# Kernel tuning notes

Measured on AMD Instinct MI355X. Metric: run time of the kernel, lower is better.

The kernel has to match this reference:

```python
import jax, jax.numpy as jnp
import numpy as np

WS = 4          # window size per axis
HEADS = 3
HEAD_DIM = 32
DIM = 96
DISP = WS // 2  # displacement for shifted windows


def _make_mask(axis):
    # (w^3, w^3) additive mask, -inf across the wrap-around boundary on `axis`
    m = np.zeros((WS, WS, WS, WS, WS, WS), dtype=np.float32)
    d = DISP
    if axis == 0:
        m[-d:, :, :, :-d, :, :] = -np.inf
        m[:-d, :, :, -d:, :, :] = -np.inf
    elif axis == 1:
        m[:, -d:, :, :, :-d, :] = -np.inf
        m[:, :-d, :, :, -d:, :] = -np.inf
    else:
        m[:, :, -d:, :, :, :-d] = -np.inf
        m[:, :, :-d, :, :, -d:] = -np.inf
    return jnp.asarray(m.reshape(WS**3, WS**3))


def setup_inputs() -> dict:
    key = jax.random.key(0)
    k1, k2, k3, k4 = jax.random.split(key, 4)
    inner = HEADS * HEAD_DIM
    x = jax.random.normal(k1, (1, 64, 64, 64, DIM), dtype=jnp.float32)
    w_qkv = jax.random.normal(k2, (3 * inner, DIM), dtype=jnp.float32) * 0.02
    w_out = jax.random.normal(k3, (DIM, inner), dtype=jnp.float32) * 0.02
    b_out = jax.random.normal(k4, (DIM,), dtype=jnp.float32) * 0.02
    return {
        'x': x, 'w_qkv': w_qkv, 'w_out': w_out, 'b_out': b_out,
        'x_mask': _make_mask(0), 'y_mask': _make_mask(1), 'z_mask': _make_mask(2),
    }


def _forward(x, w_qkv, w_out, b_out, x_mask, y_mask, z_mask):
    scale = HEAD_DIM ** -0.5
    b, nx, ny, nz, _ = x.shape
    nwx, nwy, nwz = nx // WS, ny // WS, nz // WS
    seq = WS ** 3
    # cyclic shift by -displacement
    x = jnp.roll(x, shift=(-DISP, -DISP, -DISP), axis=(1, 2, 3))
    qkv = jnp.einsum('bxyzc,oc->bxyzo', x, w_qkv)
    q, k, v = jnp.split(qkv, 3, axis=-1)

    def win(t):  # -> (b, h, n_windows, seq, d)
        t = t.reshape(b, nwx, WS, nwy, WS, nwz, WS, HEADS, HEAD_DIM)
        t = t.transpose(0, 7, 1, 3, 5, 2, 4, 6, 8)
        return t.reshape(b, HEADS, nwx * nwy * nwz, seq, HEAD_DIM)

    q, k, v = win(q), win(k), win(v)
    dots = jnp.einsum('bhwid,bhwjd->bhwij', q, k) * scale

    # shifted-window masking (faithful to original einops relabeling, incl.
    # the final mislabeled rearrange which permutes the window grid)
    d = dots.reshape(b, HEADS, nwx, nwy, nwz, seq, seq)
    d = d.transpose(0, 1, 3, 4, 2, 5, 6)          # (b,h,ny,nz,nx,i,j)
    d = d.at[:, :, :, :, -1].add(x_mask)
    d = d.transpose(0, 1, 4, 3, 2, 5, 6)          # (b,h,nx,nz,ny,i,j)
    d = d.at[:, :, :, :, -1].add(y_mask)
    d = d.transpose(0, 1, 2, 4, 3, 5, 6)          # (b,h,nx,ny,nz,i,j)
    d = d.transpose(0, 1, 4, 2, 3, 5, 6)          # original's final rearrange bug
    dots = d.reshape(b, HEADS, nwx * nwy * nwz, seq, seq)

    attn = jax.nn.softmax(dots, axis=-1)
    out = jnp.einsum('bhwij,bhwjd->bhwid', attn, v)
    # un-window
    out = out.reshape(b, HEADS, nwx, nwy, nwz, WS, WS, WS, HEAD_DIM)
    out = out.transpose(0, 2, 5, 3, 6, 4, 7, 1, 8).reshape(b, nx, ny, nz, HEADS * HEAD_DIM)
    out = jnp.einsum('bxyzc,oc->bxyzo', out, w_out) + b_out
    # cyclic back shift
    return jnp.roll(out, shift=(DISP, DISP, DISP), axis=(1, 2, 3))


def reference(x, w_qkv, w_out, b_out, x_mask, y_mask, z_mask):
    return _forward(x, w_qkv, w_out, b_out, x_mask, y_mask, z_mask)
```

## Files before the change

kernel.cpp:

```cpp
#include <hip/hip_runtime.h>
#include <hip/hip_bf16.h>


using bf4   = __attribute__((ext_vector_type(4))) short;
using bf8   = __attribute__((ext_vector_type(8))) short;
using f32x4 = __attribute__((ext_vector_type(4))) float;

#define SW      104
#define WQ_ROWS 288
#define W_ROWS  384
#define W_SHORTS (W_ROWS * SW)

__device__ __forceinline__ short f2b(float f) {
  __hip_bfloat16 h = __float2bfloat16(f);
  return *reinterpret_cast<short*>(&h);
}
__device__ __forceinline__ bf4 pk4(const f32x4& a) {
  bf4 s; s[0] = f2b(a[0]); s[1] = f2b(a[1]); s[2] = f2b(a[2]); s[3] = f2b(a[3]);
  return s;
}
__device__ __forceinline__ bf4 pk4s(const f32x4& a, float sc) {
  bf4 s; s[0] = f2b(a[0] * sc); s[1] = f2b(a[1] * sc);
  s[2] = f2b(a[2] * sc); s[3] = f2b(a[3] * sc);
  return s;
}
__device__ __forceinline__ bf8 cvt8(const float4& a, const float4& b) {
  bf8 o;
  o[0] = f2b(a.x); o[1] = f2b(a.y); o[2] = f2b(a.z); o[3] = f2b(a.w);
  o[4] = f2b(b.x); o[5] = f2b(b.y); o[6] = f2b(b.z); o[7] = f2b(b.w);
  return o;
}

#if __has_builtin(__builtin_amdgcn_mfma_f32_16x16x16bf16_1k)
__device__ __forceinline__ f32x4 mfma16(bf4 a, bf4 b, f32x4 c) {
  return __builtin_amdgcn_mfma_f32_16x16x16bf16_1k(a, b, c, 0, 0, 0);
}
#elif __has_builtin(__builtin_amdgcn_mfma_f32_16x16x16_bf16)
__device__ __forceinline__ f32x4 mfma16(bf4 a, bf4 b, f32x4 c) {
  return __builtin_amdgcn_mfma_f32_16x16x16_bf16(a, b, c, 0, 0, 0);
}
#else
__device__ __forceinline__ f32x4 mfma16(bf4 a, bf4 b, f32x4 c) {
  asm("v_mfma_f32_16x16x16_bf16 %0, %1, %2, %0" : "+v"(c) : "v"(a), "v"(b));
  return c;
}
#endif

__global__ void prep_weights(const float* __restrict__ wq, const float* __restrict__ wo,
                             short* __restrict__ wpk) {
  int i = blockIdx.x * 256 + threadIdx.x;
  if (i >= W_SHORTS) return;
  int row = i / SW, c = i - row * SW;
  const float QS = 0.17677669529663687f;
  float v = 0.f;
  if (c < 96) {
    if (row < 96)           v = wq[row * 96 + c] * QS;
    else if (row < WQ_ROWS) v = wq[row * 96 + c];
    else                    v = wo[(row - WQ_ROWS) * 96 + c];
  }
  wpk[i] = f2b(v);
}

__global__ __launch_bounds__(512, 2)
void fused_swin3d(const float* __restrict__ x,
                  const short* __restrict__ wpk,
                  const float* __restrict__ bo,
                  float* __restrict__ out) {
  __shared__ __align__(16) short ls_w[W_SHORTS];

  const int tid = threadIdx.x;
  const float4* wsrc = reinterpret_cast<const float4*>(wpk);
  #pragma unroll
  for (int i = 0; i < 10; ++i) {
    int c = i * 512 + tid;
    if (c < W_SHORTS / 8)
      *reinterpret_cast<float4*>(&ls_w[c * 8]) = wsrc[c];
  }

  const int w = (int)blockIdx.x * 8 + (tid >> 6);
  const int p = w >> 8, q = (w >> 4) & 15, r = w & 15;
  const int lane = tid & 63;
  const int lr   = lane & 15;
  const int kg   = lane >> 4;
  const int sy = (lr >> 2) & 3, sz = lr & 3;
  const int ch0 = kg * 8;
  const short* ls_wo = ls_w + WQ_ROWS * SW;

  __syncthreads();

  bf4 qn[4][6], kn[4][6], vn[4][6];
  #pragma unroll
  for (int sc = 0; sc < 4; ++sc) {
    const int gx1 = (q * 4 + sc + 2) & 63, gy1 = (r * 4 + sy + 2) & 63, gz1 = (p * 4 + sz + 2) & 63;
    const int gx2 = (p * 4 + sc + 2) & 63, gy2 = (q * 4 + sy + 2) & 63, gz2 = (r * 4 + sz + 2) & 63;
    const size_t b1 = (size_t)((gx1 * 64 + gy1) * 64 + gz1) * 96;
    const size_t b2 = (size_t)((gx2 * 64 + gy2) * 64 + gz2) * 96;

    float4 xa0 = *reinterpret_cast<const float4*>(&x[b1 +  0 + ch0]);
    float4 xa1 = *reinterpret_cast<const float4*>(&x[b1 + 32 + ch0]);
    float4 xa2 = *reinterpret_cast<const float4*>(&x[b1 + 64 + ch0]);
    float4 xa3 = *reinterpret_cast<const float4*>(&x[b1 +  0 + ch0 + 4]);
    float4 xa4 = *reinterpret_cast<const float4*>(&x[b1 + 32 + ch0 + 4]);
    float4 xa5 = *reinterpret_cast<const float4*>(&x[b1 + 64 + ch0 + 4]);
    float4 xb0 = *reinterpret_cast<const float4*>(&x[b2 +  0 + ch0]);
    float4 xb1 = *reinterpret_cast<const float4*>(&x[b2 + 32 + ch0]);
    float4 xb2 = *reinterpret_cast<const float4*>(&x[b2 + 64 + ch0]);
    float4 xb3 = *reinterpret_cast<const float4*>(&x[b2 +  0 + ch0 + 4]);
    float4 xb4 = *reinterpret_cast<const float4*>(&x[b2 + 32 + ch0 + 4]);
    float4 xb5 = *reinterpret_cast<const float4*>(&x[b2 + 64 + ch0 + 4]);

    bf8 x1[3], x2[3];
    x1[0] = cvt8(xa0, xa3); x1[1] = cvt8(xa1, xa4); x1[2] = cvt8(xa2, xa5);
    x2[0] = cvt8(xb0, xb3); x2[1] = cvt8(xb1, xb4); x2[2] = cvt8(xb2, xb5);

    #pragma unroll
    for (int n = 0; n < 12; ++n) {
      f32x4 acc = {0.f, 0.f, 0.f, 0.f};
      const short* wrow = &ls_w[(n * 16 + lr) * SW + ch0];
      acc = __builtin_amdgcn_mfma_f32_16x16x32_bf16(*reinterpret_cast<const bf8*>(wrow +  0), x1[0], acc, 0, 0, 0);
      acc = __builtin_amdgcn_mfma_f32_16x16x32_bf16(*reinterpret_cast<const bf8*>(wrow + 32), x1[1], acc, 0, 0, 0);
      acc = __builtin_amdgcn_mfma_f32_16x16x32_bf16(*reinterpret_cast<const bf8*>(wrow + 64), x1[2], acc, 0, 0, 0);
      if (n < 6) qn[sc][n] = pk4(acc);
      else       kn[sc][n - 6] = pk4(acc);
    }
    #pragma unroll
    for (int n = 0; n < 6; ++n) {
      f32x4 acc = {0.f, 0.f, 0.f, 0.f};
      const short* wrow = &ls_w[(192 + n * 16 + lr) * SW + ch0];
      acc = __builtin_amdgcn_mfma_f32_16x16x32_bf16(x2[0], *reinterpret_cast<const bf8*>(wrow +  0), acc, 0, 0, 0);
      acc = __builtin_amdgcn_mfma_f32_16x16x32_bf16(x2[1], *reinterpret_cast<const bf8*>(wrow + 32), acc, 0, 0, 0);
      acc = __builtin_amdgcn_mfma_f32_16x16x32_bf16(x2[2], *reinterpret_cast<const bf8*>(wrow + 64), acc, 0, 0, 0);
      vn[sc][n] = pk4(acc);
    }
  }

  const bool mx = (q == 15), my = (r == 15);
  const bool killy = my && ((lr >= 8) != (kg >= 2));
  bf4 ob[4][6];

  #pragma unroll
  for (int qc = 0; qc < 4; ++qc) {
    f32x4 osw[6];
    #pragma unroll
    for (int c = 0; c < 6; ++c) osw[c] = (f32x4){0.f, 0.f, 0.f, 0.f};

    #pragma unroll
    for (int h = 0; h < 3; ++h) {
      f32x4 sv[4];
      #pragma unroll
      for (int nj = 0; nj < 4; ++nj) {
        f32x4 z = {0.f, 0.f, 0.f, 0.f};
        z = mfma16(kn[nj][2 * h + 0], qn[qc][2 * h + 0], z);
        sv[nj] = mfma16(kn[nj][2 * h + 1], qn[qc][2 * h + 1], z);
      }
      float sum = 0.f;
      #pragma unroll
      for (int nj = 0; nj < 4; ++nj) {
        const bool kill = killy || (mx && ((qc >= 2) != (nj >= 2)));
        #pragma unroll
        for (int t = 0; t < 4; ++t) {
          float ev = kill ? 0.f : __expf(sv[nj][t]);
          sv[nj][t] = ev;
          sum += ev;
        }
      }
      sum += __shfl_xor(sum, 16);
      sum += __shfl_xor(sum, 32);
      const float inv = 1.f / sum;
      bf4 pb[4];
      #pragma unroll
      for (int t = 0; t < 4; ++t) pb[t] = pk4s(sv[t], inv);
      #pragma unroll
      for (int nc = 0; nc < 2; ++nc)
        #pragma unroll
        for (int t = 0; t < 4; ++t)
          osw[2 * h + nc] = mfma16(vn[t][2 * h + nc], pb[t], osw[2 * h + nc]);
    }
    #pragma unroll
    for (int c = 0; c < 6; ++c) ob[qc][c] = pk4(osw[c]);
  }

  #pragma unroll
  for (int no = 0; no < 6; ++no) {
    bf4 wa[6];
    #pragma unroll
    for (int c = 0; c < 6; ++c)
      wa[c] = *reinterpret_cast<const bf4*>(&ls_wo[(no * 16 + lr) * SW + c * 16 + kg * 4]);
    const float4 bb = *reinterpret_cast<const float4*>(&bo[no * 16 + kg * 4]);
    #pragma unroll
    for (int qc = 0; qc < 4; ++qc) {
      f32x4 acc = {0.f, 0.f, 0.f, 0.f};
      #pragma unroll
      for (int c = 0; c < 6; ++c) acc = mfma16(wa[c], ob[qc][c], acc);
      const int gx2 = (p * 4 + qc + 2) & 63, gy2 = (q * 4 + sy + 2) & 63, gz2 = (r * 4 + sz + 2) & 63;
      const size_t b2 = (size_t)((gx2 * 64 + gy2) * 64 + gz2) * 96;
      float4 o4;
      o4.x = acc[0] + bb.x; o4.y = acc[1] + bb.y;
      o4.z = acc[2] + bb.z; o4.w = acc[3] + bb.w;
      *reinterpret_cast<float4*>(&out[b2 + no * 16 + kg * 4]) = o4;
    }
  }
}

extern "C" void kernel_launch(void* const* d_in, const int* in_sizes, int n_in,
                              void* d_out, int out_size, void* d_ws, size_t ws_size,
                              hipStream_t stream) {
  const float* x  = (const float*)d_in[0];
  const float* wq = (const float*)d_in[1];
  const float* wo = (const float*)d_in[2];
  const float* bo = (const float*)d_in[3];

  short* wpk = (short*)d_ws;

  prep_weights<<<(W_SHORTS + 255) / 256, 256, 0, stream>>>(wq, wo, wpk);
  fused_swin3d<<<512, 512, 0, stream>>>(x, wpk, bo, (float*)d_out);
}
```

Before: 109.2 us.

## Batch x loads per window and reuse weight fragments across spatial chunks

Each wave now issues all x loads for its four spatial chunks up front, then loops over output tiles and reuses each weight fragment read from LDS across the four chunks instead of rereading it per chunk. Blocks shrink from 512 to 256 threads with twice as many blocks, and the LDS row stride drops from 104 to 100 shorts. The intent is better memory-level parallelism and fewer LDS reads, and it also lowers LDS footprint per block so more blocks fit per CU. The cost is much higher register pressure from holding 24 float4 loads at once, which risks spills or lower occupancy.

```diff
diff --git a/kernel.cpp b/kernel.cpp
--- a/kernel.cpp
+++ b/kernel.cpp
@@ -6,7 +6,7 @@
 using bf8   = __attribute__((ext_vector_type(8))) short;
 using f32x4 = __attribute__((ext_vector_type(4))) float;
 
-#define SW      104
+#define SW      100
 #define WQ_ROWS 288
 #define W_ROWS  384
 #define W_SHORTS (W_ROWS * SW)
@@ -61,7 +61,8 @@
   wpk[i] = f2b(v);
 }
 
-__global__ __launch_bounds__(512, 2)
+__global__ __launch_bounds__(256)
+__attribute__((amdgpu_waves_per_eu(1, 2)))
 void fused_swin3d(const float* __restrict__ x,
                   const short* __restrict__ wpk,
                   const float* __restrict__ bo,
@@ -71,13 +72,13 @@
   const int tid = threadIdx.x;
   const float4* wsrc = reinterpret_cast<const float4*>(wpk);
   #pragma unroll
-  for (int i = 0; i < 10; ++i) {
-    int c = i * 512 + tid;
+  for (int i = 0; i < 19; ++i) {
+    int c = i * 256 + tid;
     if (c < W_SHORTS / 8)
       *reinterpret_cast<float4*>(&ls_w[c * 8]) = wsrc[c];
   }
 
-  const int w = (int)blockIdx.x * 8 + (tid >> 6);
+  const int w = (int)blockIdx.x * 4 + (tid >> 6);
   const int p = w >> 8, q = (w >> 4) & 15, r = w & 15;
   const int lane = tid & 63;
   const int lr   = lane & 15;
@@ -89,48 +90,76 @@
   __syncthreads();
 
   bf4 qn[4][6], kn[4][6], vn[4][6];
-  #pragma unroll
-  for (int sc = 0; sc < 4; ++sc) {
-    const int gx1 = (q * 4 + sc + 2) & 63, gy1 = (r * 4 + sy + 2) & 63, gz1 = (p * 4 + sz + 2) & 63;
-    const int gx2 = (p * 4 + sc + 2) & 63, gy2 = (q * 4 + sy + 2) & 63, gz2 = (r * 4 + sz + 2) & 63;
-    const size_t b1 = (size_t)((gx1 * 64 + gy1) * 64 + gz1) * 96;
-    const size_t b2 = (size_t)((gx2 * 64 + gy2) * 64 + gz2) * 96;
-
-    float4 xa0 = *reinterpret_cast<const float4*>(&x[b1 +  0 + ch0]);
-    float4 xa1 = *reinterpret_cast<const float4*>(&x[b1 + 32 + ch0]);
-    float4 xa2 = *reinterpret_cast<const float4*>(&x[b1 + 64 + ch0]);
-    float4 xa3 = *reinterpret_cast<const float4*>(&x[b1 +  0 + ch0 + 4]);
-    float4 xa4 = *reinterpret_cast<const float4*>(&x[b1 + 32 + ch0 + 4]);
-    float4 xa5 = *reinterpret_cast<const float4*>(&x[b1 + 64 + ch0 + 4]);
-    float4 xb0 = *reinterpret_cast<const float4*>(&x[b2 +  0 + ch0]);
-    float4 xb1 = *reinterpret_cast<const float4*>(&x[b2 + 32 + ch0]);
-    float4 xb2 = *reinterpret_cast<const float4*>(&x[b2 + 64 + ch0]);
-    float4 xb3 = *reinterpret_cast<const float4*>(&x[b2 +  0 + ch0 + 4]);
-    float4 xb4 = *reinterpret_cast<const float4*>(&x[b2 + 32 + ch0 + 4]);
-    float4 xb5 = *reinterpret_cast<const float4*>(&x[b2 + 64 + ch0 + 4]);
-
-    bf8 x1[3], x2[3];
-    x1[0] = cvt8(xa0, xa3); x1[1] = cvt8(xa1, xa4); x1[2] = cvt8(xa2, xa5);
-    x2[0] = cvt8(xb0, xb3); x2[1] = cvt8(xb1, xb4); x2[2] = cvt8(xb2, xb5);
+
+  {
+    float4 xf[4][6];
+    #pragma unroll
+    for (int sc = 0; sc < 4; ++sc) {
+      const int gx1 = (q * 4 + sc + 2) & 63, gy1 = (r * 4 + sy + 2) & 63, gz1 = (p * 4 + sz + 2) & 63;
+      const size_t b1 = (size_t)((gx1 * 64 + gy1) * 64 + gz1) * 96;
+      #pragma unroll
+      for (int f = 0; f < 3; ++f) {
+        xf[sc][f]     = *reinterpret_cast<const float4*>(&x[b1 + f * 32 + ch0]);
+        xf[sc][3 + f] = *reinterpret_cast<const float4*>(&x[b1 + f * 32 + ch0 + 4]);
+      }
+    }
+    bf8 x1[4][3];
+    #pragma unroll
+    for (int sc = 0; sc < 4; ++sc)
+      #pragma unroll
+      for (int f = 0; f < 3; ++f) x1[sc][f] = cvt8(xf[sc][f], xf[sc][3 + f]);
 
     #pragma unroll
     for (int n = 0; n < 12; ++n) {
-      f32x4 acc = {0.f, 0.f, 0.f, 0.f};
       const short* wrow = &ls_w[(n * 16 + lr) * SW + ch0];
-      acc = __builtin_amdgcn_mfma_f32_16x16x32_bf16(*reinterpret_cast<const bf8*>(wrow +  0), x1[0], acc, 0, 0, 0);
-      acc = __builtin_amdgcn_mfma_f32_16x16x32_bf16(*reinterpret_cast<const bf8*>(wrow + 32), x1[1], acc, 0, 0, 0);
-      acc = __builtin_amdgcn_mfma_f32_16x16x32_bf16(*reinterpret_cast<const bf8*>(wrow + 64), x1[2], acc, 0, 0, 0);
-      if (n < 6) qn[sc][n] = pk4(acc);
-      else       kn[sc][n - 6] = pk4(acc);
-    }
+      const bf8 w0 = *reinterpret_cast<const bf8*>(wrow +  0);
+      const bf8 w1 = *reinterpret_cast<const bf8*>(wrow + 32);
+      const bf8 w2 = *reinterpret_cast<const bf8*>(wrow + 64);
+      #pragma unroll
+      for (int sc = 0; sc < 4; ++sc) {
+        f32x4 acc = {0.f, 0.f, 0.f, 0.f};
+        acc = __builtin_amdgcn_mfma_f32_16x16x32_bf16(w0, x1[sc][0], acc, 0, 0, 0);
+        acc = __builtin_amdgcn_mfma_f32_16x16x32_bf16(w1, x1[sc][1], acc, 0, 0, 0);
+        acc = __builtin_amdgcn_mfma_f32_16x16x32_bf16(w2, x1[sc][2], acc, 0, 0, 0);
+        if (n < 6) qn[sc][n] = pk4(acc);
+        else       kn[sc][n - 6] = pk4(acc);
+      }
+    }
+  }
+
+  size_t b2s[4];
+  {
+    float4 xf[4][6];
+    #pragma unroll
+    for (int sc = 0; sc < 4; ++sc) {
+      const int gx2 = (p * 4 + sc + 2) & 63, gy2 = (q * 4 + sy + 2) & 63, gz2 = (r * 4 + sz + 2) & 63;
+      b2s[sc] = (size_t)((gx2 * 64 + gy2) * 64 + gz2) * 96;
+      #pragma unroll
+      for (int f = 0; f < 3; ++f) {
+        xf[sc][f]     = *reinterpret_cast<const float4*>(&x[b2s[sc] + f * 32 + ch0]);
+        xf[sc][3 + f] = *reinterpret_cast<const float4*>(&x[b2s[sc] + f * 32 + ch0 + 4]);
+      }
+    }
+    bf8 x2[4][3];
+    #pragma unroll
+    for (int sc = 0; sc < 4; ++sc)
+      #pragma unroll
+      for (int f = 0; f < 3; ++f) x2[sc][f] = cvt8(xf[sc][f], xf[sc][3 + f]);
+
     #pragma unroll
     for (int n = 0; n < 6; ++n) {
-      f32x4 acc = {0.f, 0.f, 0.f, 0.f};
       const short* wrow = &ls_w[(192 + n * 16 + lr) * SW + ch0];
-      acc = __builtin_amdgcn_mfma_f32_16x16x32_bf16(x2[0], *reinterpret_cast<const bf8*>(wrow +  0), acc, 0, 0, 0);
-      acc = __builtin_amdgcn_mfma_f32_16x16x32_bf16(x2[1], *reinterpret_cast<const bf8*>(wrow + 32), acc, 0, 0, 0);
-      acc = __builtin_amdgcn_mfma_f32_16x16x32_bf16(x2[2], *reinterpret_cast<const bf8*>(wrow + 64), acc, 0, 0, 0);
-      vn[sc][n] = pk4(acc);
+      const bf8 w0 = *reinterpret_cast<const bf8*>(wrow +  0);
+      const bf8 w1 = *reinterpret_cast<const bf8*>(wrow + 32);
+      const bf8 w2 = *reinterpret_cast<const bf8*>(wrow + 64);
+      #pragma unroll
+      for (int sc = 0; sc < 4; ++sc) {
+        f32x4 acc = {0.f, 0.f, 0.f, 0.f};
+        acc = __builtin_amdgcn_mfma_f32_16x16x32_bf16(x2[sc][0], w0, acc, 0, 0, 0);
+        acc = __builtin_amdgcn_mfma_f32_16x16x32_bf16(x2[sc][1], w1, acc, 0, 0, 0);
+        acc = __builtin_amdgcn_mfma_f32_16x16x32_bf16(x2[sc][2], w2, acc, 0, 0, 0);
+        vn[sc][n] = pk4(acc);
+      }
     }
   }
 
@@ -192,12 +221,10 @@
       f32x4 acc = {0.f, 0.f, 0.f, 0.f};
       #pragma unroll
       for (int c = 0; c < 6; ++c) acc = mfma16(wa[c], ob[qc][c], acc);
-      const int gx2 = (p * 4 + qc + 2) & 63, gy2 = (q * 4 + sy + 2) & 63, gz2 = (r * 4 + sz + 2) & 63;
-      const size_t b2 = (size_t)((gx2 * 64 + gy2) * 64 + gz2) * 96;
       float4 o4;
       o4.x = acc[0] + bb.x; o4.y = acc[1] + bb.y;
       o4.z = acc[2] + bb.z; o4.w = acc[3] + bb.w;
-      *reinterpret_cast<float4*>(&out[b2 + no * 16 + kg * 4]) = o4;
+      *reinterpret_cast<float4*>(&out[b2s[qc] + no * 16 + kg * 4]) = o4;
     }
   }
 }
@@ -213,5 +240,5 @@
   short* wpk = (short*)d_ws;
 
   prep_weights<<<(W_SHORTS + 255) / 256, 256, 0, stream>>>(wq, wo, wpk);
-  fused_swin3d<<<512, 512, 0, stream>>>(x, wpk, bo, (float*)d_out);
-}
+  fused_swin3d<<<1024, 256, 0, stream>>>(x, wpk, bo, (float*)d_out);
+}
```

Measured after the change: 102.6 us. 1.06x faster.
